# Kernel optimization log

Hardware: AMD Instinct MI355X
Metric: run time of the kernel (lower is better)

The kernel has to match this reference:

```python
import jax, jax.numpy as jnp
import numpy as np

S, B = 64, 16          # seq_len, batch
V = 32000              # ntoken
NINP = 512             # ninp (embedding / decoder input dim)
NHID = 1536            # nhid (intermediate LSTM layers)
NHL = 1024             # nhidlast (last LSTM layer)
E = 8                  # n_experts


def setup_inputs() -> dict:
    key = jax.random.key(0)
    ks = jax.random.split(key, 24)

    def unif(k, shape, r=0.1):
        return jax.random.uniform(k, shape, jnp.float32, -r, r)

    inp = {
        "tokens": jax.random.randint(ks[0], (S, B), 0, V),
        "h0": jnp.zeros((B, NHID), jnp.float32),
        "c0": jnp.zeros((B, NHID), jnp.float32),
        "h1": jnp.zeros((B, NHID), jnp.float32),
        "c1": jnp.zeros((B, NHID), jnp.float32),
        "h2": jnp.zeros((B, NHL), jnp.float32),
        "c2": jnp.zeros((B, NHL), jnp.float32),
        # parameters
        "emb": unif(ks[1], (V, NINP)),
        "Wih0": unif(ks[2], (4 * NHID, NINP)),
        "Whh0": unif(ks[3], (4 * NHID, NHID)),
        "b0": jnp.zeros((4 * NHID,), jnp.float32),
        "Wih1": unif(ks[4], (4 * NHID, NHID)),
        "Whh1": unif(ks[5], (4 * NHID, NHID)),
        "b1": jnp.zeros((4 * NHID,), jnp.float32),
        "Wih2": unif(ks[6], (4 * NHL, NHID)),
        "Whh2": unif(ks[7], (4 * NHL, NHL)),
        "b2": jnp.zeros((4 * NHL,), jnp.float32),
        "prior_W": unif(ks[8], (E, NHL)),
        "latent_W": unif(ks[9], (E * NINP, NHL)),
        "latent_b": jnp.zeros((E * NINP,), jnp.float32),
        "dec_W": unif(ks[10], (V, NINP)),
        "dec_b": jnp.zeros((V,), jnp.float32),
        "gain": jnp.ones((NINP,), jnp.float32),   # decoder_gain (frozen ones)
    }
    return inp


def _lstm_layer(x, h0, c0, Wih, Whh, b):
    # x: (S, B, Din); gate order i, f, g, o as in torch
    xg = jnp.einsum('sbd,gd->sbg', x, Wih) + b  # precompute input projections

    def step(carry, xt):
        h, c = carry
        g = xt + h @ Whh.T
        i, f, gg, o = jnp.split(g, 4, axis=-1)
        c = jax.nn.sigmoid(f) * c + jax.nn.sigmoid(i) * jnp.tanh(gg)
        h = jax.nn.sigmoid(o) * jnp.tanh(c)
        return (h, c), h

    (hT, cT), ys = jax.lax.scan(step, (h0, c0), xg)
    return ys, hT, cT


def reference(tokens, h0, c0, h1, c1, h2, c2, emb, Wih0, Whh0, b0,
              Wih1, Whh1, b1, Wih2, Whh2, b2, prior_W, latent_W, latent_b,
              dec_W, dec_b, gain):
    x = emb[tokens]                                   # (S, B, NINP)
    x, _, _ = _lstm_layer(x, h0, c0, Wih0, Whh0, b0)  # (S, B, NHID)
    x, _, _ = _lstm_layer(x, h1, c1, Wih1, Whh1, b1)  # (S, B, NHID)
    out, _, _ = _lstm_layer(x, h2, c2, Wih2, Whh2, b2)  # (S, B, NHL)

    # MoS head
    latent = jnp.tanh(jnp.einsum('sbh,eh->sbe', out, latent_W) + latent_b)
    latent = latent.reshape(S * B * E, NINP)          # (S*B*E, NINP)
    logit = (latent * gain) @ dec_W.T + dec_b         # (S*B*E, V)
    prior = jax.nn.softmax(out.reshape(S * B, NHL) @ prior_W.T, axis=-1)  # (S*B, E)
    prob = jax.nn.softmax(logit, axis=-1).reshape(S * B, E, V)
    prob = jnp.einsum('nev,ne->nv', prob, prior)      # mixture over experts
    log_prob = jnp.log(prob + 1e-8)
    return log_prob.reshape(S, B, V)
```

## Files before the change

kernel.cpp:

```cpp
#include <hip/hip_runtime.h>
#include <hip/hip_bf16.h>

typedef __attribute__((ext_vector_type(8))) short short8;
typedef __attribute__((ext_vector_type(4))) float f32x4;
typedef unsigned short u16;
typedef unsigned long long u64;

__device__ __forceinline__ u16 f2b(float f) {
    unsigned u = __float_as_uint(f);
    return (u16)((u + 0x7FFFu + ((u >> 16) & 1u)) >> 16);
}
__device__ __forceinline__ float b2f(u16 u) {
    return __uint_as_float(((unsigned)u) << 16);
}
__device__ __forceinline__ void gload16(const void* g, void* l) {
    __builtin_amdgcn_global_load_lds(
        (const __attribute__((address_space(1))) void*)g,
        (__attribute__((address_space(3))) void*)l, 16, 0, 0);
}

struct CvtJobs {
    const float* s[6];
    u16* d[6];
    int n4[6];
    int njobs;
};

__global__ __launch_bounds__(256)
void k_f2b(const float* __restrict__ s, u16* __restrict__ d, int n4)
{
    int i = blockIdx.x * 256 + threadIdx.x;
    if (i >= n4) return;
    float4 v = ((const float4*)s)[i];
    short4 o;
    o.x = (short)f2b(v.x); o.y = (short)f2b(v.y);
    o.z = (short)f2b(v.z); o.w = (short)f2b(v.w);
    ((short4*)d)[i] = o;
}

__global__ __launch_bounds__(256)
void k_embed(const int* __restrict__ tok, const float* __restrict__ emb,
             u16* __restrict__ x0)
{
    int i = blockIdx.x * 256 + threadIdx.x;
    int n = i >> 7, p4 = i & 127;
    float4 v = ((const float4*)(emb + (size_t)tok[n] * 512))[p4];
    short4 o;
    o.x = (short)f2b(v.x); o.y = (short)f2b(v.y);
    o.z = (short)f2b(v.z); o.w = (short)f2b(v.w);
    ((short4*)x0)[i] = o;
}

template <int EPI>
__global__ __launch_bounds__(256)
void k_gemm(const u16* __restrict__ A, const u16* __restrict__ B,
            const float* __restrict__ bias, void* __restrict__ Cp,
            int M, int N, int K, const float* __restrict__ gain,
            float* __restrict__ rsum)
{
    __shared__ __align__(16) u16 As[2][128 * 32];
    __shared__ __align__(16) u16 Bs[2][128 * 32];
    __shared__ float rs[2][128];
    const int tid = threadIdx.x;
    const int lane = tid & 63, wid = tid >> 6;
    const int wr = wid >> 1, wc = wid & 1;
    const int l15 = lane & 15, l4 = lane >> 4;
    const int row0 = blockIdx.y * 128, col0 = blockIdx.x * 128;

    const int srA = wid * 16 + (lane >> 2);
    const int skA = (lane & 3) * 8;

    auto stage = [&](int buf, int k0) {
        gload16(A + (size_t)(row0 + srA) * K + k0 + skA, &As[buf][wid * 512]);
        gload16(A + (size_t)(row0 + 64 + srA) * K + k0 + skA, &As[buf][2048 + wid * 512]);
        gload16(B + (size_t)(col0 + srA) * K + k0 + skA, &Bs[buf][wid * 512]);
        gload16(B + (size_t)(col0 + 64 + srA) * K + k0 + skA, &Bs[buf][2048 + wid * 512]);
    };

    f32x4 acc[4][4] = {};

    stage(0, 0);
    __syncthreads();
    int cur = 0;
    for (int k0 = 0; k0 < K; k0 += 32) {
        if (k0 + 32 < K) stage(cur ^ 1, k0 + 32);

        short8 af[4], bfv[4];
#pragma unroll
        for (int i = 0; i < 4; ++i)
            af[i]  = *(const short8*)&As[cur][(wr * 64 + i * 16 + l15) * 32 + l4 * 8];
#pragma unroll
        for (int i = 0; i < 4; ++i)
            bfv[i] = *(const short8*)&Bs[cur][(wc * 64 + i * 16 + l15) * 32 + l4 * 8];
#pragma unroll
        for (int mi = 0; mi < 4; ++mi)
#pragma unroll
            for (int ni = 0; ni < 4; ++ni)
                acc[mi][ni] = __builtin_amdgcn_mfma_f32_16x16x32_bf16(
                    af[mi], bfv[ni], acc[mi][ni], 0, 0, 0);
        __syncthreads();
        cur ^= 1;
    }

    if (EPI == 2) {
#pragma unroll
        for (int mi = 0; mi < 4; ++mi) {
#pragma unroll
            for (int j = 0; j < 4; ++j) {
                int rb = row0 + wr * 64 + mi * 16 + l4 * 4 + j;
                float rsub = 0.f;
#pragma unroll
                for (int ni = 0; ni < 4; ++ni) {
                    int cc = col0 + wc * 64 + ni * 16 + l15;
                    float pv = expf(fminf(acc[mi][ni][j] + bias[cc], 80.f));
                    ((u16*)Cp)[(size_t)rb * N + cc] = f2b(pv);
                    rsub += pv;
                }
#pragma unroll
                for (int o = 1; o < 16; o <<= 1) rsub += __shfl_xor(rsub, o, 64);
                if (l15 == 0)
                    rs[wc][wr * 64 + mi * 16 + l4 * 4 + j] = rsub;
            }
        }
        __syncthreads();
        if (tid < 128)
            atomicAdd(&rsum[row0 + tid], rs[0][tid] + rs[1][tid]);
        return;
    }

#pragma unroll
    for (int mi = 0; mi < 4; ++mi) {
#pragma unroll
        for (int ni = 0; ni < 4; ++ni) {
            int rb = row0 + wr * 64 + mi * 16 + l4 * 4;
            int cc = col0 + wc * 64 + ni * 16 + l15;
            float bv = bias[cc];
#pragma unroll
            for (int j = 0; j < 4; ++j) {
                float v = acc[mi][ni][j] + bv;
                if (EPI == 0) {
                    ((float*)Cp)[(size_t)(rb + j) * N + cc] = v;
                } else {
                    int e = cc >> 9, pp = cc & 511;
                    ((u16*)Cp)[(((size_t)(rb + j) * 8 + e) << 9) | pp] =
                        f2b(tanhf(v) * gain[pp]);
                }
            }
        }
    }
}

__global__ __launch_bounds__(512)
void k_gemm_dec(const u16* __restrict__ A, const u16* __restrict__ B,
                const float* __restrict__ bias, u16* __restrict__ pe,
                int M, int N, int K, float* __restrict__ rsum)
{
    __shared__ __align__(16) u16 As[2][256 * 32];
    __shared__ __align__(16) u16 Bs[2][128 * 32];
    __shared__ float rs[2][256];
    const int tid = threadIdx.x;
    const int lane = tid & 63, wid = tid >> 6;
    const int wr = wid >> 1, wc = wid & 1;
    const int l15 = lane & 15, l4 = lane >> 4;
    const int row0 = blockIdx.y * 256, col0 = blockIdx.x * 128;

    const int srA = wid * 16 + (lane >> 2);
    const int skA = (lane & 3) * 8;

    auto stage = [&](int buf, int k0) {
        gload16(A + (size_t)(row0 + srA) * K + k0 + skA, &As[buf][wid * 512]);
        gload16(A + (size_t)(row0 + 128 + srA) * K + k0 + skA, &As[buf][4096 + wid * 512]);
        gload16(B + (size_t)(col0 + srA) * K + k0 + skA, &Bs[buf][wid * 512]);
    };

    f32x4 acc[4][4] = {};

    stage(0, 0);
    __syncthreads();
    int cur = 0;
    for (int k0 = 0; k0 < K; k0 += 32) {
        if (k0 + 32 < K) stage(cur ^ 1, k0 + 32);

        short8 af[4], bfv[4];
#pragma unroll
        for (int i = 0; i < 4; ++i)
            af[i]  = *(const short8*)&As[cur][(wr * 64 + i * 16 + l15) * 32 + l4 * 8];
#pragma unroll
        for (int i = 0; i < 4; ++i)
            bfv[i] = *(const short8*)&Bs[cur][(wc * 64 + i * 16 + l15) * 32 + l4 * 8];
#pragma unroll
        for (int mi = 0; mi < 4; ++mi)
#pragma unroll
            for (int ni = 0; ni < 4; ++ni)
                acc[mi][ni] = __builtin_amdgcn_mfma_f32_16x16x32_bf16(
                    af[mi], bfv[ni], acc[mi][ni], 0, 0, 0);
        __syncthreads();
        cur ^= 1;
    }

#pragma unroll
    for (int mi = 0; mi < 4; ++mi) {
#pragma unroll
        for (int j = 0; j < 4; ++j) {
            int rloc = wr * 64 + mi * 16 + l4 * 4 + j;
            float rsub = 0.f;
#pragma unroll
            for (int ni = 0; ni < 4; ++ni) {
                int cc = col0 + wc * 64 + ni * 16 + l15;
                float pv = expf(fminf(acc[mi][ni][j] + bias[cc], 80.f));
                pe[(size_t)(row0 + rloc) * N + cc] = f2b(pv);
                rsub += pv;
            }
#pragma unroll
            for (int o = 1; o < 16; o <<= 1) rsub += __shfl_xor(rsub, o, 64);
            if (l15 == 0) rs[wc][rloc] = rsub;
        }
    }
    __syncthreads();
    if (tid < 256)
        atomicAdd(&rsum[row0 + tid], rs[0][tid] + rs[1][tid]);
}

template <int DH>
__global__ void __launch_bounds__(512)
k_rnn(const float* __restrict__ xg,
      const u16* __restrict__ W,
      const float* __restrict__ h0f,
      const float* __restrict__ c0f,
      u16* __restrict__ y,
      unsigned* __restrict__ bar,
      int nb, CvtJobs jobs)
{
    if ((int)blockIdx.x >= nb) {
        const int hb = blockIdx.x - nb, nh = gridDim.x - nb;
        for (int j = 0; j < jobs.njobs; ++j) {
            const float4* s = (const float4*)jobs.s[j];
            short4* d = (short4*)jobs.d[j];
            const int n4 = jobs.n4[j];
            for (int i = hb * 512 + threadIdx.x; i < n4; i += nh * 512) {
                float4 v = s[i];
                short4 o;
                o.x = (short)f2b(v.x); o.y = (short)f2b(v.y);
                o.z = (short)f2b(v.z); o.w = (short)f2b(v.w);
                d[i] = o;
            }
        }
        return;
    }

    constexpr int DH2 = DH / 2;
    constexpr int NSH = DH2 / 32;
    constexpr int NL  = 16 * DH / 4 / 512;
    constexpr int RW  = DH / 4;
    constexpr int LDH = DH + 8;
    __shared__ __align__(16) u16 hs[16][LDH];
    __shared__ __align__(16) f32x4 red[8][64];
    __shared__ __align__(16) u16 hout[16][16];

    const int tid = threadIdx.x;
    const int lane = tid & 63, wid = tid >> 6;
    const int g = wid & 3, kh = wid >> 2;
    const int l15 = lane & 15, l4 = lane >> 4;
    const int u0 = blockIdx.x * 16;

    short8 wfr[NSH];
    {
        const u16* wa = W + (size_t)(g * DH + u0 + l15) * DH + kh * DH2 + l4 * 8;
#pragma unroll
        for (int s = 0; s < NSH; ++s) wfr[s] = *(const short8*)(wa + s * 32);
    }

    const int eb = tid >> 4, eu = tid & 15;
    float c_reg = (tid < 256) ? c0f[(size_t)eb * DH + u0 + eu] : 0.f;

    for (int t = 0; t < 64; ++t) {
        float xpre[4];
        if (tid < 256) {
            const float* xr = xg + (size_t)(t * 16 + eb) * 4 * DH + u0 + eu;
#pragma unroll
            for (int gg = 0; gg < 4; ++gg) xpre[gg] = xr[(size_t)gg * DH];
        }

        if (t == 0) {
            for (int i = tid; i < 16 * DH / 4; i += 512) {
                int r = i / (DH / 4), k4 = i % (DH / 4);
                float4 v = *(const float4*)(h0f + (size_t)r * DH + k4 * 4);
                short4 o;
                o.x = (short)f2b(v.x); o.y = (short)f2b(v.y);
                o.z = (short)f2b(v.z); o.w = (short)f2b(v.w);
                *(short4*)&hs[r][k4 * 4] = o;
            }
            __syncthreads();
        } else {
            if (tid < nb) {
                while (__hip_atomic_load(bar + tid * 32, __ATOMIC_RELAXED,
                                         __HIP_MEMORY_SCOPE_AGENT) < (unsigned)t)
                    __builtin_amdgcn_s_sleep(1);
            }
            __syncthreads();
            const u64* hp = (const u64*)(y + (size_t)(t - 1) * 16 * DH);
            u64 tmp[NL];
#pragma unroll
            for (int j = 0; j < NL; ++j)
                tmp[j] = __hip_atomic_load(hp + tid + j * 512, __ATOMIC_RELAXED,
                                           __HIP_MEMORY_SCOPE_AGENT);
#pragma unroll
            for (int j = 0; j < NL; ++j) {
                int idx = tid + j * 512;
                int r = idx / RW, c = (idx % RW) * 4;
                *(u64*)&hs[r][c] = tmp[j];
            }
            __syncthreads();
        }

        f32x4 acc = {};
#pragma unroll
        for (int s = 0; s < NSH; ++s) {
            short8 hf = *(const short8*)&hs[l15][kh * DH2 + s * 32 + l4 * 8];
            acc = __builtin_amdgcn_mfma_f32_16x16x32_bf16(hf, wfr[s], acc, 0, 0, 0);
        }
        red[wid][lane] = acc;
        __syncthreads();

        if (tid < 256) {
            const int li = (eb >> 2) * 16 + eu, j = eb & 3;
            float gt[4];
#pragma unroll
            for (int gg = 0; gg < 4; ++gg)
                gt[gg] = ((const float*)&red[gg][li])[j]
                       + ((const float*)&red[4 + gg][li])[j]
                       + xpre[gg];
            float si = 1.f / (1.f + expf(-gt[0]));
            float sf = 1.f / (1.f + expf(-gt[1]));
            float so = 1.f / (1.f + expf(-gt[3]));
            c_reg = sf * c_reg + si * tanhf(gt[2]);
            hout[eb][eu] = f2b(so * tanhf(c_reg));
        }
        __syncthreads();

        if (tid < 64) {
            int r = tid >> 2, c4 = (tid & 3) * 4;
            u64 v = *(const u64*)&hout[r][c4];
            __hip_atomic_store((u64*)(y + (size_t)(t * 16 + r) * DH + u0 + c4), v,
                               __ATOMIC_RELAXED, __HIP_MEMORY_SCOPE_AGENT);
        }

        if (t < 63) {
            __syncthreads();
            if (tid == 0)
                __hip_atomic_store(bar + blockIdx.x * 32, (unsigned)(t + 1),
                                   __ATOMIC_RELAXED, __HIP_MEMORY_SCOPE_AGENT);
        }
    }
}

__global__ __launch_bounds__(256)
void k_prior(const u16* __restrict__ out2, const float* __restrict__ pW,
             float* __restrict__ prior)
{
    const int n = blockIdx.x;
    const int tid = threadIdx.x;
    const int e = tid >> 5, lane = tid & 31;
    const u16* x = out2 + (size_t)n * 1024;
    const float* w = pW + (size_t)e * 1024;
    float s = 0.f;
    for (int k = lane; k < 1024; k += 32) s += b2f(x[k]) * w[k];
#pragma unroll
    for (int o = 16; o; o >>= 1) s += __shfl_down(s, o, 32);
    __shared__ float es[8];
    if (lane == 0) es[e] = s;
    __syncthreads();
    if (tid == 0) {
        float m = -1e30f;
        for (int i = 0; i < 8; ++i) m = fmaxf(m, es[i]);
        float Z = 0.f, ex[8];
        for (int i = 0; i < 8; ++i) { ex[i] = expf(es[i] - m); Z += ex[i]; }
        for (int i = 0; i < 8; ++i) prior[(size_t)n * 8 + i] = ex[i] / Z;
    }
}

__global__ __launch_bounds__(128)
void k_combine(const u16* __restrict__ pe, const float* __restrict__ prior,
               const float* __restrict__ rsum, float* __restrict__ out, int n0)
{
    const int v2 = blockIdx.x * 128 + threadIdx.x;
    const int nl = blockIdx.y;
    __shared__ float w[8];
    if (threadIdx.x < 8)
        w[threadIdx.x] = prior[(size_t)(n0 + nl) * 8 + threadIdx.x]
                       / rsum[nl * 8 + threadIdx.x];
    __syncthreads();
    float a0 = 0.f, a1 = 0.f;
#pragma unroll
    for (int e = 0; e < 8; ++e) {
        unsigned pv = *(const unsigned*)&pe[(size_t)(nl * 8 + e) * 32000 + v2 * 2];
        a0 += b2f((u16)(pv & 0xffff)) * w[e];
        a1 += b2f((u16)(pv >> 16)) * w[e];
    }
    float2 o;
    o.x = logf(a0 + 1e-8f);
    o.y = logf(a1 + 1e-8f);
    *(float2*)&out[(size_t)(n0 + nl) * 32000 + v2 * 2] = o;
}

extern "C" void kernel_launch(void* const* d_in, const int* in_sizes, int n_in,
                              void* d_out, int out_size, void* d_ws, size_t ws_size,
                              hipStream_t stream)
{
    const int*   tok  = (const int*)d_in[0];
    const float* h0   = (const float*)d_in[1];
    const float* c0   = (const float*)d_in[2];
    const float* h1   = (const float*)d_in[3];
    const float* c1   = (const float*)d_in[4];
    const float* h2   = (const float*)d_in[5];
    const float* c2   = (const float*)d_in[6];
    const float* emb  = (const float*)d_in[7];
    const float* Wih0 = (const float*)d_in[8];
    const float* Whh0 = (const float*)d_in[9];
    const float* b0   = (const float*)d_in[10];
    const float* Wih1 = (const float*)d_in[11];
    const float* Whh1 = (const float*)d_in[12];
    const float* b1   = (const float*)d_in[13];
    const float* Wih2 = (const float*)d_in[14];
    const float* Whh2 = (const float*)d_in[15];
    const float* b2   = (const float*)d_in[16];
    const float* priW = (const float*)d_in[17];
    const float* latW = (const float*)d_in[18];
    const float* latb = (const float*)d_in[19];
    const float* decW = (const float*)d_in[20];
    const float* decb = (const float*)d_in[21];
    const float* gain = (const float*)d_in[22];

    char* p = (char*)d_ws;
    auto alloc = [&](size_t bytes) {
        char* r = p; p += (bytes + 255) & ~(size_t)255; return r;
    };
    u16* Whh0b = (u16*)alloc(6144ull * 1536 * 2);
    u16* Whh1b = (u16*)alloc(6144ull * 1536 * 2);
    u16* Whh2b = (u16*)alloc(4096ull * 1024 * 2);
    u16* latWb = (u16*)alloc(4096ull * 1024 * 2);
    u16* decWb = (u16*)alloc(32000ull * 512 * 2);
    u16* latb16 = (u16*)alloc(8192ull * 512 * 2);
    float* pri   = (float*)alloc(8192 * 4);
    float* rowsum = (float*)alloc(8192 * 4);
    u16* out2 = (u16*)alloc(1024ull * 1024 * 2);
    unsigned* bars = (unsigned*)alloc(3 * 96 * 32 * 4);
    char* trans = p;
    u16* Wih0b = (u16*)alloc(6144ull * 512 * 2);
    u16* Wih1b = (u16*)alloc(6144ull * 1536 * 2);
    u16* Wih2b = (u16*)alloc(4096ull * 1536 * 2);
    u16* x0 = (u16*)alloc(1024ull * 512 * 2);
    u16* x1 = (u16*)alloc(1024ull * 1536 * 2);
    u16* x2 = (u16*)alloc(1024ull * 1536 * 2);
    float* xg = (float*)alloc(1024ull * 6144 * 4);
    u16* pe = (u16*)trans;
    size_t cap = ws_size - (size_t)(trans - (char*)d_ws);
    int chunkRows = 128;
    if (cap >= 1024ull * 32000 * 2) chunkRows = 1024;
    else if (cap >= 512ull * 32000 * 2) chunkRows = 512;
    else if (cap >= 256ull * 32000 * 2) chunkRows = 256;
    int nPer = chunkRows / 8;

    hipMemsetAsync(bars, 0, 3 * 96 * 32 * 4, stream);
    hipMemsetAsync(rowsum, 0, 8192 * 4, stream);

    k_f2b<<<9216, 256, 0, stream>>>(Whh0, Whh0b, 2359296);
    k_f2b<<<3072, 256, 0, stream>>>(Wih0, Wih0b, 786432);
    k_embed<<<512, 256, 0, stream>>>(tok, emb, x0);

    k_gemm<0><<<dim3(48, 8), 256, 0, stream>>>(
        x0, Wih0b, b0, xg, 1024, 6144, 512, nullptr, nullptr);
    {
        unsigned* bar = bars;
        int nb = 96;
        CvtJobs jobs;
        jobs.s[0] = Whh1; jobs.d[0] = Whh1b; jobs.n4[0] = 2359296;
        jobs.s[1] = Whh2; jobs.d[1] = Whh2b; jobs.n4[1] = 1048576;
        jobs.s[2] = Wih1; jobs.d[2] = Wih1b; jobs.n4[2] = 2359296;
        jobs.s[3] = Wih2; jobs.d[3] = Wih2b; jobs.n4[3] = 1572864;
        jobs.s[4] = latW; jobs.d[4] = latWb; jobs.n4[4] = 1048576;
        jobs.s[5] = decW; jobs.d[5] = decWb; jobs.n4[5] = 4096000;
        jobs.njobs = 6;
        void* args[] = {(void*)&xg, (void*)&Whh0b, (void*)&h0, (void*)&c0,
                        (void*)&x1, (void*)&bar, (void*)&nb, (void*)&jobs};
        hipLaunchCooperativeKernel(reinterpret_cast<void*>(&k_rnn<1536>),
                                   dim3(256), dim3(512), args, 0, stream);
    }

    k_gemm<0><<<dim3(48, 8), 256, 0, stream>>>(
        x1, Wih1b, b1, xg, 1024, 6144, 1536, nullptr, nullptr);
    {
        unsigned* bar = bars + 96 * 32;
        int nb = 96;
        CvtJobs jobs;
        jobs.njobs = 0;
        void* args[] = {(void*)&xg, (void*)&Whh1b, (void*)&h1, (void*)&c1,
                        (void*)&x2, (void*)&bar, (void*)&nb, (void*)&jobs};
        hipLaunchCooperativeKernel(reinterpret_cast<void*>(&k_rnn<1536>),
                                   dim3(96), dim3(512), args, 0, stream);
    }

    k_gemm<0><<<dim3(32, 8), 256, 0, stream>>>(
        x2, Wih2b, b2, xg, 1024, 4096, 1536, nullptr, nullptr);
    {
        unsigned* bar = bars + 2 * 96 * 32;
        int nb = 64;
        CvtJobs jobs;
        jobs.njobs = 0;
        void* args[] = {(void*)&xg, (void*)&Whh2b, (void*)&h2, (void*)&c2,
                        (void*)&out2, (void*)&bar, (void*)&nb, (void*)&jobs};
        hipLaunchCooperativeKernel(reinterpret_cast<void*>(&k_rnn<1024>),
                                   dim3(64), dim3(512), args, 0, stream);
    }

    k_prior<<<1024, 256, 0, stream>>>(out2, priW, pri);
    k_gemm<1><<<dim3(32, 8), 256, 0, stream>>>(
        out2, latWb, latb, latb16, 1024, 4096, 1024, gain, nullptr);

    for (int nb = 0; nb < 1024; nb += nPer) {
        const u16* Ach = latb16 + (size_t)nb * 8 * 512;
        float* rsumc = rowsum + (size_t)nb * 8;
        if (chunkRows >= 256) {
            k_gemm_dec<<<dim3(250, chunkRows / 256), 512, 0, stream>>>(
                Ach, decWb, decb, pe, chunkRows, 32000, 512, rsumc);
        } else {
            k_gemm<2><<<dim3(250, chunkRows / 128), 256, 0, stream>>>(
                Ach, decWb, decb, pe, chunkRows, 32000, 512, nullptr, rsumc);
        }
        k_combine<<<dim3(125, nPer), 128, 0, stream>>>(
            pe, pri, rowsum + nb * 8, (float*)d_out, nb);
    }
}
```

Measured before the change: 1.426 ms.

## Overlap decoder GEMM with previous chunk's mixture combine via double-buffered logits

Double-buffers the bf16 exp-logit chunk buffer and adds an extra row of blocks to the decoder GEMM grid. Those blocks perform the expert-mixture combine and log for the previous chunk while the GEMM blocks compute the current chunk. This removes the serialized standalone combine launches except for the last chunk. In exchange it needs twice the workspace, so a smaller chunk size may be chosen. The combine blocks also compete with GEMM blocks for CUs and memory bandwidth.

```diff
diff --git a/kernel.cpp b/kernel.cpp
--- a/kernel.cpp
+++ b/kernel.cpp
@@ -153,12 +153,37 @@
 __global__ __launch_bounds__(512)
 void k_gemm_dec(const u16* __restrict__ A, const u16* __restrict__ B,
                 const float* __restrict__ bias, u16* __restrict__ pe,
-                int M, int N, int K, float* __restrict__ rsum)
+                int M, int N, int K, float* __restrict__ rsum,
+                const u16* __restrict__ pePrev, const float* __restrict__ prior,
+                const float* __restrict__ rsumPrev, float* __restrict__ outp,
+                int n0prev, int nPer)
 {
     __shared__ __align__(16) u16 As[2][256 * 32];
     __shared__ __align__(16) u16 Bs[2][128 * 32];
     __shared__ float rs[2][256];
     const int tid = threadIdx.x;
+
+    if ((int)blockIdx.y == (int)gridDim.y - 1) {
+        if (n0prev < 0) return;
+        float* wsh = (float*)As;
+        for (int i = tid; i < nPer * 8; i += 512)
+            wsh[i] = prior[(size_t)(n0prev + (i >> 3)) * 8 + (i & 7)]
+                   / rsumPrev[i];
+        __syncthreads();
+        const int total = nPer * 32000;
+        const int stride = gridDim.x * 512;
+        for (int i = blockIdx.x * 512 + tid; i < total; i += stride) {
+            int nl = i / 32000, v = i - nl * 32000;
+            float acc = 0.f;
+#pragma unroll
+            for (int e = 0; e < 8; ++e)
+                acc += b2f(pePrev[(size_t)(nl * 8 + e) * 32000 + v])
+                     * wsh[nl * 8 + e];
+            outp[(size_t)(n0prev + nl) * 32000 + v] = logf(acc + 1e-8f);
+        }
+        return;
+    }
+
     const int lane = tid & 63, wid = tid >> 6;
     const int wr = wid >> 1, wc = wid & 1;
     const int l15 = lane & 15, l4 = lane >> 4;
@@ -453,13 +478,17 @@
     u16* x1 = (u16*)alloc(1024ull * 1536 * 2);
     u16* x2 = (u16*)alloc(1024ull * 1536 * 2);
     float* xg = (float*)alloc(1024ull * 6144 * 4);
-    u16* pe = (u16*)trans;
     size_t cap = ws_size - (size_t)(trans - (char*)d_ws);
-    int chunkRows = 128;
-    if (cap >= 1024ull * 32000 * 2) chunkRows = 1024;
-    else if (cap >= 512ull * 32000 * 2) chunkRows = 512;
-    else if (cap >= 256ull * 32000 * 2) chunkRows = 256;
+    int chunkRows;
+    bool fused;
+    if      (cap >= 2ull * 1024 * 32000 * 2) { chunkRows = 1024; fused = true; }
+    else if (cap >= 2ull * 512 * 32000 * 2)  { chunkRows = 512;  fused = true; }
+    else if (cap >= 2ull * 256 * 32000 * 2)  { chunkRows = 256;  fused = true; }
+    else                                     { chunkRows = 128;  fused = false; }
     int nPer = chunkRows / 8;
+    size_t chunkElems = (size_t)chunkRows * 32000;
+    u16* pe0 = (u16*)trans;
+    u16* pe1 = pe0 + chunkElems;
 
     hipMemsetAsync(bars, 0, 3 * 96 * 32 * 4, stream);
     hipMemsetAsync(rowsum, 0, 8192 * 4, stream);
@@ -517,17 +546,32 @@
     k_gemm<1><<<dim3(32, 8), 256, 0, stream>>>(
         out2, latWb, latb, latb16, 1024, 4096, 1024, gain, nullptr);
 
-    for (int nb = 0; nb < 1024; nb += nPer) {
-        const u16* Ach = latb16 + (size_t)nb * 8 * 512;
-        float* rsumc = rowsum + (size_t)nb * 8;
-        if (chunkRows >= 256) {
-            k_gemm_dec<<<dim3(250, chunkRows / 256), 512, 0, stream>>>(
-                Ach, decWb, decb, pe, chunkRows, 32000, 512, rsumc);
-        } else {
+    if (fused) {
+        const int rowTiles = chunkRows / 256;
+        const int nChunks = 1024 / nPer;
+        for (int ci = 0; ci < nChunks; ++ci) {
+            int nb = ci * nPer;
+            u16* peCur = (ci & 1) ? pe1 : pe0;
+            const u16* pePrev = (ci & 1) ? pe0 : pe1;
+            int n0prev = nb - nPer;
+            const float* rsPrev = rowsum + (size_t)(n0prev < 0 ? 0 : n0prev) * 8;
+            k_gemm_dec<<<dim3(250, rowTiles + 1), 512, 0, stream>>>(
+                latb16 + (size_t)nb * 8 * 512, decWb, decb, peCur,
+                chunkRows, 32000, 512, rowsum + (size_t)nb * 8,
+                pePrev, pri, rsPrev, (float*)d_out, n0prev, nPer);
+        }
+        int n0t = 1024 - nPer;
+        const u16* peLast = ((nChunks - 1) & 1) ? pe1 : pe0;
+        k_combine<<<dim3(125, nPer), 128, 0, stream>>>(
+            peLast, pri, rowsum + (size_t)n0t * 8, (float*)d_out, n0t);
+    } else {
+        for (int nb = 0; nb < 1024; nb += nPer) {
+            const u16* Ach = latb16 + (size_t)nb * 8 * 512;
+            float* rsumc = rowsum + (size_t)nb * 8;
             k_gemm<2><<<dim3(250, chunkRows / 128), 256, 0, stream>>>(
-                Ach, decWb, decb, pe, chunkRows, 32000, 512, nullptr, rsumc);
-        }
-        k_combine<<<dim3(125, nPer), 128, 0, stream>>>(
-            pe, pri, rowsum + nb * 8, (float*)d_out, nb);
-    }
-}
+                Ach, decWb, decb, pe0, chunkRows, 32000, 512, nullptr, rsumc);
+            k_combine<<<dim3(125, nPer), 128, 0, stream>>>(
+                pe0, pri, rsumc, (float*)d_out, nb);
+        }
+    }
+}
```

Measured after the change: 1.424 ms, median of 2. No clear change (-0.1%).
